# Kernel tuning notes

Hardware: AMD Instinct MI355X
Metric: run time of the kernel (lower is better)

The kernel has to match this reference:

```python
import jax, jax.numpy as jnp
import numpy as np

D_MODEL = 768
D_STATE = 128
D_CONV = 4
EXPAND = 2
HEADDIM = 64
NGROUPS = 1
D_INNER = EXPAND * D_MODEL            # 1536
NHEADS = D_INNER // HEADDIM           # 24
CONV_DIM = D_INNER + 2 * NGROUPS * D_STATE  # 1792
D_IN_PROJ = 2 * D_INNER + 2 * NGROUPS * D_STATE + NHEADS  # 3352
EPS = 1e-5


def setup_inputs() -> dict:
    key = jax.random.key(0)
    ks = jax.random.split(key, 8)
    b, l = 4, 2048
    return {
        "feature": jax.random.normal(ks[0], (b, l, D_MODEL), jnp.float32),
        "in_proj_w": jax.random.normal(ks[1], (D_IN_PROJ, D_MODEL), jnp.float32) * 0.02,
        "conv_w": jax.random.normal(ks[2], (CONV_DIM, D_CONV), jnp.float32) * 0.2,
        "conv_b": jnp.zeros((CONV_DIM,), jnp.float32),
        "dt_bias": jax.random.normal(ks[3], (NHEADS,), jnp.float32) * 0.1,
        # A in [1,16) -> A_log = log(A)
        "A_log": jnp.log(1.0 + 15.0 * jax.random.uniform(ks[4], (NHEADS,), jnp.float32)),
        "D": jnp.ones((NHEADS,), jnp.float32),
        "norm_w": jnp.ones((D_INNER,), jnp.float32),
        "out_proj_w": jax.random.normal(ks[5], (D_MODEL, D_INNER), jnp.float32) * 0.02,
        "gate1": jnp.float32(0.6),
    }


def _mamba2(u, in_proj_w, conv_w, conv_b, dt_bias, A_log, D, norm_w, out_proj_w):
    b, l, _ = u.shape
    zxbcdt = jnp.einsum('bld,ed->ble', u, in_proj_w)  # [b,l,3352]
    z, xBC, dt = jnp.split(zxbcdt, [D_INNER, D_INNER + CONV_DIM], axis=-1)
    dt = jax.nn.softplus(dt + dt_bias)  # [b,l,h]

    # causal depthwise conv1d + silu on xBC
    xc = jnp.transpose(xBC, (0, 2, 1))  # [b,c,l]
    xc = jax.lax.conv_general_dilated(
        xc, conv_w[:, None, :], (1,), [(D_CONV - 1, 0)],
        dimension_numbers=('NCH', 'OIH', 'NCH'), feature_group_count=CONV_DIM)
    xBC = jax.nn.silu(jnp.transpose(xc, (0, 2, 1)) + conv_b)

    x, B, C = jnp.split(xBC, [D_INNER, D_INNER + NGROUPS * D_STATE], axis=-1)
    x = x.reshape(b, l, NHEADS, HEADDIM)
    A = -jnp.exp(A_log)          # [h], negative
    dA = jnp.exp(dt * A)         # [b,l,h]

    def step(h, inp):
        # h: [b,h,p,n]
        dA_t, dt_t, x_t, B_t, C_t = inp  # [b,h],[b,h],[b,h,p],[b,n],[b,n]
        h = h * dA_t[..., None, None] + (dt_t[..., None] * x_t)[..., None] * B_t[:, None, None, :]
        y = jnp.einsum('bhpn,bn->bhp', h, C_t)
        return h, y

    h0 = jnp.zeros((b, NHEADS, HEADDIM, D_STATE), u.dtype)
    xs = (jnp.moveaxis(dA, 1, 0), jnp.moveaxis(dt, 1, 0), jnp.moveaxis(x, 1, 0),
          jnp.moveaxis(B, 1, 0), jnp.moveaxis(C, 1, 0))
    _, ys = jax.lax.scan(step, h0, xs)           # [l,b,h,p]
    y = jnp.moveaxis(ys, 0, 1) + x * D[None, None, :, None]
    y = y.reshape(b, l, D_INNER)

    # gated RMSNorm: gate then normalize (norm_before_gate=False)
    y = y * jax.nn.silu(z)
    y = y * jax.lax.rsqrt(jnp.mean(y * y, axis=-1, keepdims=True) + EPS) * norm_w
    return jnp.einsum('bld,ed->ble', y, out_proj_w)


def reference(feature, in_proj_w, conv_w, conv_b, dt_bias, A_log, D, norm_w, out_proj_w, gate1):
    out = _mamba2(feature, in_proj_w, conv_w, conv_b, dt_bias, A_log, D, norm_w, out_proj_w)
    return jax.nn.sigmoid(gate1) * out
```

## Files before the change

### kernel.cpp

```cpp
#include <hip/hip_runtime.h>
#include <cstddef>

#define NB 4
#define SEQL 2048
#define DMODEL 768
#define DSTATE 128
#define HEADDIM 64
#define NHEADS 24
#define DINNER 1536
#define CONVDIM 1792
#define DINPROJ 3352
#define BLROWS (NB*SEQL)
#define RMS_EPS 1e-5f
#define Q 128
#define NC (SEQL/Q)
#define BOFF DINNER
#define COFF (DINNER + DSTATE)
#define BK 64

typedef unsigned int uint;
typedef unsigned short ushort;
typedef __attribute__((ext_vector_type(8))) short bf16x8;
typedef __attribute__((ext_vector_type(4))) float f32x4;

__device__ __forceinline__ float sigmoidf_(float x){ return 1.f/(1.f+expf(-x)); }
__device__ __forceinline__ float siluf_(float x){ return x * sigmoidf_(x); }
__device__ __forceinline__ float softplusf_(float x){ return x > 20.f ? x : log1pf(expf(x)); }

__device__ __forceinline__ ushort f2bf(float f){
    union { float f; uint u; } v; v.f = f;
    uint r = (v.u + 0x7FFFu + ((v.u >> 16) & 1u)) >> 16;
    return (ushort)r;
}
__device__ __forceinline__ float bf2f(ushort s){
    union { uint u; float f; } v; v.u = ((uint)s) << 16;
    return v.f;
}
__device__ __forceinline__ uint pack2(float a, float b){
    return (uint)f2bf(a) | ((uint)f2bf(b) << 16);
}
__device__ __forceinline__ void unpack8(uint4 r, float* o){
    o[0]=bf2f((ushort)(r.x&0xffff)); o[1]=bf2f((ushort)(r.x>>16));
    o[2]=bf2f((ushort)(r.y&0xffff)); o[3]=bf2f((ushort)(r.y>>16));
    o[4]=bf2f((ushort)(r.z&0xffff)); o[5]=bf2f((ushort)(r.z>>16));
    o[6]=bf2f((ushort)(r.w&0xffff)); o[7]=bf2f((ushort)(r.w>>16));
}
__device__ __forceinline__ uint packu2(ushort a, ushort b){
    return (uint)a | ((uint)b << 16);
}

#define GLD16(g, l) __builtin_amdgcn_global_load_lds( \
    (const __attribute__((address_space(1))) void*)(g), \
    (__attribute__((address_space(3))) void*)(l), 16, 0, 0)

__global__ __launch_bounds__(256) void cast_kernel(
    const float* __restrict__ in, ushort* __restrict__ out, int n4)
{
    const int i = blockIdx.x*256 + threadIdx.x;
    if (i < n4) {
        float4 v = ((const float4*)in)[i];
        ushort4 o = make_ushort4(f2bf(v.x), f2bf(v.y), f2bf(v.z), f2bf(v.w));
        ((ushort4*)out)[i] = o;
    }
}

__global__ __launch_bounds__(256) void gemm_mfma(
    const ushort* __restrict__ A, const ushort* __restrict__ W,
    float* __restrict__ C, int M, int N, int K,
    const float* __restrict__ gptr)
{
    __shared__ __align__(16) ushort sm[2*12288];
    const int tid = threadIdx.x;
    const int wv = tid >> 6, ln = tid & 63;
    const int id = blockIdx.x;
    const int xcd = id & 7;
    const int local = id >> 3;
    const int m0 = (xcd*8 + (local & 7)) * 128;
    const int n0 = (local >> 3) * 64;
    const int wm = (wv >> 1) * 64, wn = (wv & 1) * 32;

    const int sr = ln >> 3;
    const int scol = ((ln & 7) ^ sr) * 8;
    const ushort* gA[4]; ushort* lA[4];
#pragma unroll
    for (int iss = 0; iss < 4; ++iss) {
        gA[iss] = A + (size_t)(m0 + wv*32 + iss*8 + sr) * K + scol;
        lA[iss] = &sm[(wv*32 + iss*8) * BK];
    }
    const ushort* gB[2]; ushort* lB[2];
#pragma unroll
    for (int iss = 0; iss < 2; ++iss) {
        gB[iss] = W + (size_t)(n0 + wv*16 + iss*8 + sr) * K + scol;
        lB[iss] = &sm[8192 + (wv*16 + iss*8) * BK];
    }

    f32x4 acc[4][2];
#pragma unroll
    for (int i = 0; i < 4; ++i)
#pragma unroll
        for (int j = 0; j < 2; ++j) acc[i][j] = (f32x4){0.f, 0.f, 0.f, 0.f};

    const int fr = ln & 15;
    const int fq = ln >> 4;
    const int nt = K / BK;

#pragma unroll
    for (int iss = 0; iss < 4; ++iss) GLD16(gA[iss], lA[iss]);
#pragma unroll
    for (int iss = 0; iss < 2; ++iss) GLD16(gB[iss], lB[iss]);

    for (int kt = 0; kt < nt; ++kt) {
        if (kt + 1 < nt) {
            const int so = ((kt + 1) & 1) * 12288;
            const int ko = (kt + 1) * BK;
#pragma unroll
            for (int iss = 0; iss < 4; ++iss) GLD16(gA[iss] + ko, lA[iss] + so);
#pragma unroll
            for (int iss = 0; iss < 2; ++iss) GLD16(gB[iss] + ko, lB[iss] + so);
            asm volatile("s_waitcnt vmcnt(6)" ::: "memory");
        } else {
            asm volatile("s_waitcnt vmcnt(0)" ::: "memory");
        }
        __builtin_amdgcn_s_barrier();
        const ushort* As = sm + (kt & 1) * 12288;
        const ushort* Bs = As + 8192;
#pragma unroll
        for (int kh = 0; kh < 2; ++kh) {
            const int sw = ((kh*4 + fq) ^ (fr & 7)) * 8;
            bf16x8 af[4], bfr[2];
#pragma unroll
            for (int i = 0; i < 4; ++i)
                af[i] = *(const bf16x8*)&As[(wm + i*16 + fr)*BK + sw];
#pragma unroll
            for (int j = 0; j < 2; ++j)
                bfr[j] = *(const bf16x8*)&Bs[(wn + j*16 + fr)*BK + sw];
#pragma unroll
            for (int i = 0; i < 4; ++i)
#pragma unroll
                for (int j = 0; j < 2; ++j)
                    acc[i][j] = __builtin_amdgcn_mfma_f32_16x16x32_bf16(af[i], bfr[j], acc[i][j], 0, 0, 0);
        }
        __builtin_amdgcn_s_barrier();
    }

    float scale = 1.f;
    if (gptr) scale = sigmoidf_(*gptr);
    const int cn = ln & 15;
    const int cr = (ln >> 4) * 4;
#pragma unroll
    for (int i = 0; i < 4; ++i) {
        const int mb = m0 + wm + i*16 + cr;
#pragma unroll
        for (int j = 0; j < 2; ++j) {
            const int n = n0 + wn + j*16 + cn;
            if (n < N) {
                float* cp = C + (size_t)mb * N + n;
                cp[0*(size_t)N] = acc[i][j].x * scale;
                cp[1*(size_t)N] = acc[i][j].y * scale;
                cp[2*(size_t)N] = acc[i][j].z * scale;
                cp[3*(size_t)N] = acc[i][j].w * scale;
            }
        }
    }
}

__global__ __launch_bounds__(256) void gemm_mfma_bf16o(
    const ushort* __restrict__ A, const ushort* __restrict__ W,
    ushort* __restrict__ C, float* __restrict__ dtraw, int M, int N, int K)
{
    __shared__ __align__(16) ushort sm[2*128*BK*2];
    const int tid = threadIdx.x;
    const int wv = tid >> 6, ln = tid & 63;
    const int id = blockIdx.x;
    const int xcd = id & 7;
    const int local = id >> 3;
    const int m0 = (xcd*8 + (local & 7)) * 128;
    const int n0 = (local >> 3) * 128;
    const int wm = (wv >> 1) * 64, wn = (wv & 1) * 64;

    const int sr = ln >> 3;
    const int scol = ((ln & 7) ^ sr) * 8;
    const ushort* gA[4]; const ushort* gB[4];
    ushort* lA[4]; ushort* lB[4];
#pragma unroll
    for (int iss = 0; iss < 4; ++iss) {
        const int ra = m0 + wv*32 + iss*8 + sr;
        gA[iss] = A + (size_t)ra * K + scol;
        int rb = n0 + wv*32 + iss*8 + sr; if (rb >= N) rb = N - 1;
        gB[iss] = W + (size_t)rb * K + scol;
        lA[iss] = &sm[(wv*32 + iss*8) * BK];
        lB[iss] = &sm[8192 + (wv*32 + iss*8) * BK];
    }

    f32x4 acc[4][4];
#pragma unroll
    for (int i = 0; i < 4; ++i)
#pragma unroll
        for (int j = 0; j < 4; ++j) acc[i][j] = (f32x4){0.f, 0.f, 0.f, 0.f};

    const int fr = ln & 15;
    const int fq = ln >> 4;
    const int nt = K / BK;

#pragma unroll
    for (int iss = 0; iss < 4; ++iss) {
        GLD16(gA[iss], lA[iss]);
        GLD16(gB[iss], lB[iss]);
    }

    for (int kt = 0; kt < nt; ++kt) {
        if (kt + 1 < nt) {
            const int so = ((kt + 1) & 1) * 16384;
            const int ko = (kt + 1) * BK;
#pragma unroll
            for (int iss = 0; iss < 4; ++iss) {
                GLD16(gA[iss] + ko, lA[iss] + so);
                GLD16(gB[iss] + ko, lB[iss] + so);
            }
            asm volatile("s_waitcnt vmcnt(8)" ::: "memory");
        } else {
            asm volatile("s_waitcnt vmcnt(0)" ::: "memory");
        }
        __builtin_amdgcn_s_barrier();
        const ushort* As = sm + (kt & 1) * 16384;
        const ushort* Bs = As + 8192;
#pragma unroll
        for (int kh = 0; kh < 2; ++kh) {
            const int sw = ((kh*4 + fq) ^ (fr & 7)) * 8;
            bf16x8 af[4], bfr[4];
#pragma unroll
            for (int i = 0; i < 4; ++i)
                af[i] = *(const bf16x8*)&As[(wm + i*16 + fr)*BK + sw];
#pragma unroll
            for (int j = 0; j < 4; ++j)
                bfr[j] = *(const bf16x8*)&Bs[(wn + j*16 + fr)*BK + sw];
#pragma unroll
            for (int i = 0; i < 4; ++i)
#pragma unroll
                for (int j = 0; j < 4; ++j)
                    acc[i][j] = __builtin_amdgcn_mfma_f32_16x16x32_bf16(af[i], bfr[j], acc[i][j], 0, 0, 0);
        }
        __builtin_amdgcn_s_barrier();
    }

    const int cn = ln & 15;
    const int cr = (ln >> 4) * 4;
    __syncthreads();
    ushort* rp = sm + wv*4096;
#pragma unroll
    for (int i = 0; i < 4; ++i)
#pragma unroll
        for (int j = 0; j < 4; ++j) {
            const int colb = j*16 + cn;
#pragma unroll
            for (int r = 0; r < 4; ++r) {
                const int row = i*16 + cr + r;
                rp[row*64 + (((colb >> 3) ^ (row & 7)) * 8) + (colb & 7)] = f2bf(acc[i][j][r]);
            }
        }
    __syncthreads();
#pragma unroll
    for (int k2 = 0; k2 < 8; ++k2) {
        const int row = k2*8 + (ln >> 3);
        const int cg = ln & 7;
        uint4 v = *(const uint4*)&rp[row*64 + ((cg ^ (row & 7)) * 8)];
        const int gm = m0 + wm + row;
        const int gn = n0 + wn + cg*8;
        if (gn + 8 <= N)
            *(uint4*)(C + (size_t)gm*N + gn) = v;
    }
    if (n0 + 128 > N) {
#pragma unroll
        for (int i = 0; i < 4; ++i) {
            const int mb = m0 + wm + i*16 + cr;
#pragma unroll
            for (int j = 0; j < 4; ++j) {
                const int col = (n0 + wn + j*16 + cn) - (N - 24);
                if (col >= 0 && col < 24) {
                    dtraw[(size_t)(mb+0)*24 + col] = acc[i][j].x;
                    dtraw[(size_t)(mb+1)*24 + col] = acc[i][j].y;
                    dtraw[(size_t)(mb+2)*24 + col] = acc[i][j].z;
                    dtraw[(size_t)(mb+3)*24 + col] = acc[i][j].w;
                }
            }
        }
    }
}

__global__ __launch_bounds__(448) void conv_kernel(
    const ushort* __restrict__ zx, const float* __restrict__ conv_w,
    const float* __restrict__ conv_b, ushort* __restrict__ xconv)
{
    const int c4 = threadIdx.x;
    const int bl0 = blockIdx.x * 16;
    const int l0 = bl0 & (SEQL - 1);
    float w[4][4];
#pragma unroll
    for (int j = 0; j < 4; ++j) {
        float4 wr = *(const float4*)(conv_w + (c4*4 + j)*4);
        w[j][0]=wr.x; w[j][1]=wr.y; w[j][2]=wr.z; w[j][3]=wr.w;
    }
    const float4 bias = *(const float4*)(conv_b + c4*4);
    const ushort* src = zx + DINNER + (size_t)c4*4;
    ushort* dst = xconv + (size_t)c4*4;

    float h0[4], h1[4], h2[4];
    if (l0 == 0) {
#pragma unroll
        for (int ch = 0; ch < 4; ++ch) { h0[ch]=0.f; h1[ch]=0.f; h2[ch]=0.f; }
    } else {
        ushort4 a = *(const ushort4*)(src + (size_t)(bl0-3)*DINPROJ);
        ushort4 b = *(const ushort4*)(src + (size_t)(bl0-2)*DINPROJ);
        ushort4 c = *(const ushort4*)(src + (size_t)(bl0-1)*DINPROJ);
        h0[0]=bf2f(a.x); h0[1]=bf2f(a.y); h0[2]=bf2f(a.z); h0[3]=bf2f(a.w);
        h1[0]=bf2f(b.x); h1[1]=bf2f(b.y); h1[2]=bf2f(b.z); h1[3]=bf2f(b.w);
        h2[0]=bf2f(c.x); h2[1]=bf2f(c.y); h2[2]=bf2f(c.z); h2[3]=bf2f(c.w);
    }
#pragma unroll
    for (int t = 0; t < 16; ++t) {
        ushort4 xv = *(const ushort4*)(src + (size_t)(bl0 + t)*DINPROJ);
        float h3[4] = {bf2f(xv.x), bf2f(xv.y), bf2f(xv.z), bf2f(xv.w)};
        float s0 = fmaf(h3[0], w[0][3], fmaf(h2[0], w[0][2], fmaf(h1[0], w[0][1], fmaf(h0[0], w[0][0], bias.x))));
        float s1 = fmaf(h3[1], w[1][3], fmaf(h2[1], w[1][2], fmaf(h1[1], w[1][1], fmaf(h0[1], w[1][0], bias.y))));
        float s2 = fmaf(h3[2], w[2][3], fmaf(h2[2], w[2][2], fmaf(h1[2], w[2][1], fmaf(h0[2], w[2][0], bias.z))));
        float s3 = fmaf(h3[3], w[3][3], fmaf(h2[3], w[3][2], fmaf(h1[3], w[3][1], fmaf(h0[3], w[3][0], bias.w))));
        ushort4 o = make_ushort4(f2bf(siluf_(s0)), f2bf(siluf_(s1)),
                                 f2bf(siluf_(s2)), f2bf(siluf_(s3)));
        *(ushort4*)(dst + (size_t)(bl0 + t)*CONVDIM) = o;
#pragma unroll
        for (int ch = 0; ch < 4; ++ch) { h0[ch]=h1[ch]; h1[ch]=h2[ch]; h2[ch]=h3[ch]; }
    }
}

__global__ __launch_bounds__(128) void dtscan_kernel(
    const float* __restrict__ dtraw, const float* __restrict__ dt_bias,
    const float* __restrict__ A_log, float* __restrict__ dtc, float* __restrict__ clog)
{
    const int c = blockIdx.x, h = blockIdx.y, b = blockIdx.z;
    const int t = threadIdx.x;
    const int bl = b*SEQL + c*Q + t;
    float draw = dtraw[(size_t)bl*24 + h] + dt_bias[h];
    float dtv = softplusf_(draw);
    float la = -expf(A_log[h]) * dtv;
    const int lane = t & 63;
    float v = la;
#pragma unroll
    for (int off = 1; off < 64; off <<= 1) {
        float u = __shfl_up(v, off);
        if (lane >= off) v += u;
    }
    __shared__ float w0tot;
    if (t == 63) w0tot = v;
    __syncthreads();
    if (t >= 64) v += w0tot;
    const int idx = (b*NHEADS + h)*SEQL + c*Q + t;
    dtc[idx] = dtv;
    clog[idx] = v;
}

__global__ __launch_bounds__(256) void gcb_mfma(
    const ushort* __restrict__ xconv, ushort* __restrict__ G)
{
    __shared__ __align__(16) ushort Ca[64*32];
    __shared__ __align__(16) ushort Bb[128*32];
    const int thalf = blockIdx.x, c = blockIdx.y, b = blockIdx.z;
    const int tid = threadIdx.x;
    const int wv = tid >> 6, ln = tid & 63;
    const int fr = ln & 15, fq = ln >> 4, fk = fq*8;
    const int bl0 = b*SEQL + c*Q;
    const int th0 = thalf*64;

    const int sat = tid & 63,  sac = (tid >> 6)*8;
    const int sbt = tid & 127, sbh = (tid >> 7)*16;

    f32x4 acc[4][2];
#pragma unroll
    for (int i = 0; i < 4; ++i)
#pragma unroll
        for (int j = 0; j < 2; ++j) acc[i][j] = (f32x4){0.f,0.f,0.f,0.f};

    for (int ks = 0; ks < 4; ++ks) {
        uint4 av = *(const uint4*)(xconv + (size_t)(bl0 + th0 + sat)*CONVDIM + COFF + ks*32 + sac);
        const ushort* br = xconv + (size_t)(bl0 + sbt)*CONVDIM + BOFF + ks*32 + sbh;
        uint4 bv0 = *(const uint4*)br;
        uint4 bv1 = *(const uint4*)(br + 8);
        __syncthreads();
        *(uint4*)&Ca[sat*32 + sac] = av;
        *(uint4*)&Bb[sbt*32 + sbh] = bv0;
        *(uint4*)&Bb[sbt*32 + sbh + 8] = bv1;
        __syncthreads();
        bf16x8 av_[4], bv_[2];
#pragma unroll
        for (int i = 0; i < 4; ++i)
            av_[i] = *(const bf16x8*)&Ca[(i*16 + fr)*32 + fk];
#pragma unroll
        for (int j = 0; j < 2; ++j)
            bv_[j] = *(const bf16x8*)&Bb[(wv*32 + j*16 + fr)*32 + fk];
#pragma unroll
        for (int i = 0; i < 4; ++i)
#pragma unroll
            for (int j = 0; j < 2; ++j)
                acc[i][j] = __builtin_amdgcn_mfma_f32_16x16x32_bf16(av_[i], bv_[j], acc[i][j], 0, 0, 0);
    }
    ushort* gout = G + (size_t)(b*NC + c)*(Q*Q);
#pragma unroll
    for (int i = 0; i < 4; ++i) {
#pragma unroll
        for (int j = 0; j < 2; ++j) {
            const int s = wv*32 + j*16 + fr;
#pragma unroll
            for (int r = 0; r < 4; ++r) {
                const int t = th0 + i*16 + fq*4 + r;
                gout[t*Q + s] = f2bf(acc[i][j][r]);
            }
        }
    }
}

#define ASTR 40
#define BSTR 40
__global__ __launch_bounds__(256) void locstate_mfma(
    const ushort* __restrict__ xconv, const float* __restrict__ dtc,
    const float* __restrict__ clog, ushort* __restrict__ Sloc)
{
    __shared__ __align__(16) ushort Ab[64*ASTR];
    __shared__ __align__(16) ushort Bb[128*BSTR];
    __shared__ float sw[Q];
    const int c = blockIdx.x, h = blockIdx.y, b = blockIdx.z;
    const int tid = threadIdx.x;
    const int wv = tid >> 6, ln = tid & 63;
    const int fr = ln & 15, fq = ln >> 4, fk = fq*8;
    const int bh = b*NHEADS + h;
    const int bl0 = b*SEQL + c*Q;

    if (tid < Q) {
        const float ce = clog[(size_t)bh*SEQL + c*Q + (Q-1)];
        const float cs = clog[(size_t)bh*SEQL + c*Q + tid];
        sw[tid] = dtc[(size_t)bh*SEQL + c*Q + tid] * expf(ce - cs);
    }
    __syncthreads();

    f32x4 acc[4][2];
#pragma unroll
    for (int i = 0; i < 4; ++i)
#pragma unroll
        for (int j = 0; j < 2; ++j) acc[i][j] = (f32x4){0.f,0.f,0.f,0.f};

    const int ap = tid & 63, aoct = tid >> 6;
    const int bn = tid & 127, bhalf = tid >> 7;

    for (int ks = 0; ks < 4; ++ks) {
        float xv[8];
#pragma unroll
        for (int j = 0; j < 8; ++j) {
            const int s = ks*32 + aoct*8 + j;
            xv[j] = bf2f(xconv[(size_t)(bl0 + s)*CONVDIM + h*HEADDIM + ap]) * sw[s];
        }
        ushort bu[16];
#pragma unroll
        for (int j = 0; j < 16; ++j) {
            const int s = ks*32 + bhalf*16 + j;
            bu[j] = xconv[(size_t)(bl0 + s)*CONVDIM + BOFF + bn];
        }
        __syncthreads();
        *(uint4*)&Ab[ap*ASTR + aoct*8] =
            make_uint4(pack2(xv[0],xv[1]), pack2(xv[2],xv[3]),
                       pack2(xv[4],xv[5]), pack2(xv[6],xv[7]));
        *(uint4*)&Bb[bn*BSTR + bhalf*16] =
            make_uint4(packu2(bu[0],bu[1]), packu2(bu[2],bu[3]),
                       packu2(bu[4],bu[5]), packu2(bu[6],bu[7]));
        *(uint4*)&Bb[bn*BSTR + bhalf*16 + 8] =
            make_uint4(packu2(bu[8],bu[9]), packu2(bu[10],bu[11]),
                       packu2(bu[12],bu[13]), packu2(bu[14],bu[15]));
        __syncthreads();
        bf16x8 af[4], bf[2];
#pragma unroll
        for (int i = 0; i < 4; ++i)
            af[i] = *(const bf16x8*)&Ab[(i*16 + fr)*ASTR + fk];
#pragma unroll
        for (int j = 0; j < 2; ++j)
            bf[j] = *(const bf16x8*)&Bb[(wv*32 + j*16 + fr)*BSTR + fk];
#pragma unroll
        for (int i = 0; i < 4; ++i)
#pragma unroll
            for (int j = 0; j < 2; ++j)
                acc[i][j] = __builtin_amdgcn_mfma_f32_16x16x32_bf16(af[i], bf[j], acc[i][j], 0, 0, 0);
    }
    ushort* dst = Sloc + (size_t)((b*NC + c)*NHEADS + h) * (HEADDIM*DSTATE);
#pragma unroll
    for (int i = 0; i < 4; ++i) {
#pragma unroll
        for (int j = 0; j < 2; ++j) {
            const int n = wv*32 + j*16 + fr;
#pragma unroll
            for (int r = 0; r < 4; ++r) {
                const int p = i*16 + fq*4 + r;
                dst[p*DSTATE + n] = f2bf(acc[i][j][r]);
            }
        }
    }
}

__global__ __launch_bounds__(256) void chunkscan_kernel(
    const float* __restrict__ clog, ushort* __restrict__ S)
{
    const int h = blockIdx.x, b = blockIdx.y, pg = blockIdx.z;
    const int tid = threadIdx.x;
    const int p = pg*16 + (tid >> 4);
    const int n0 = (tid & 15) * 8;
    const int bh = b*NHEADS + h;
    float st[8];
#pragma unroll
    for (int j = 0; j < 8; ++j) st[j] = 0.f;

    for (int c = 0; c < NC; ++c) {
        const float tc = expf(clog[(size_t)bh*SEQL + c*Q + (Q-1)]);
        ushort* base = S + (size_t)((b*NC + c)*NHEADS + h) * (HEADDIM*DSTATE);
        uint4 raw = *(uint4*)(base + p*DSTATE + n0);
        float lv[8];
        unpack8(raw, lv);
        uint4 pre = make_uint4(pack2(st[0],st[1]), pack2(st[2],st[3]),
                               pack2(st[4],st[5]), pack2(st[6],st[7]));
        *(uint4*)(base + p*DSTATE + n0) = pre;
#pragma unroll
        for (int j = 0; j < 8; ++j) st[j] = fmaf(tc, st[j], lv[j]);
    }
}

__global__ __launch_bounds__(256) void ychunk_mfma(
    const ushort* __restrict__ xconv, const float* __restrict__ dtc,
    const float* __restrict__ clog, const ushort* __restrict__ G,
    const ushort* __restrict__ Sp, const float* __restrict__ Dv,
    ushort* __restrict__ ybf)
{
    __shared__ __align__(16) ushort smu[8192];
    ushort* Ab = smu;
    ushort* Bb = smu + 4096;
    __shared__ float s_clog[Q];
    __shared__ float s_dtc[Q];
    const int c = blockIdx.x, h = blockIdx.y, b = blockIdx.z;
    const int tid = threadIdx.x;
    const int wv = tid >> 6, ln = tid & 63;
    const int bh = b*NHEADS + h;
    const int bl0 = b*SEQL + c*Q;
    const int fr = ln & 15, fq = ln >> 4, fk = fq*8;

    if (tid < Q) {
        s_clog[tid] = clog[(size_t)bh*SEQL + c*Q + tid];
        s_dtc[tid]  = dtc [(size_t)bh*SEQL + c*Q + tid];
    }

    f32x4 acc[2][4];
#pragma unroll
    for (int i = 0; i < 2; ++i)
#pragma unroll
        for (int j = 0; j < 4; ++j) acc[i][j] = (f32x4){0.f,0.f,0.f,0.f};

    const int sgt = tid & 127, sgh = (tid >> 7)*16;
    const int sbp = tid & 63,  sbc = (tid >> 6)*8;
    const ushort* spb = Sp + (size_t)((b*NC + c)*NHEADS + h)*(HEADDIM*DSTATE);

    for (int ks = 0; ks < 4; ++ks) {
        const ushort* cr = xconv + (size_t)(bl0 + sgt)*CONVDIM + COFF + ks*32 + sgh;
        uint4 cv0 = *(const uint4*)cr;
        uint4 cv1 = *(const uint4*)(cr + 8);
        uint4 sv = *(const uint4*)(spb + sbp*DSTATE + ks*32 + sbc);
        __syncthreads();
        *(uint4*)&Ab[sgt*32 + sgh]     = cv0;
        *(uint4*)&Ab[sgt*32 + sgh + 8] = cv1;
        *(uint4*)&Bb[sbp*32 + sbc] = sv;
        __syncthreads();
        bf16x8 af[2], bv[4];
        af[0] = *(const bf16x8*)&Ab[(wv*32 +      fr)*32 + fk];
        af[1] = *(const bf16x8*)&Ab[(wv*32 + 16 + fr)*32 + fk];
#pragma unroll
        for (int j = 0; j < 4; ++j)
            bv[j] = *(const bf16x8*)&Bb[(j*16 + fr)*32 + fk];
#pragma unroll
        for (int i = 0; i < 2; ++i)
#pragma unroll
            for (int j = 0; j < 4; ++j)
                acc[i][j] = __builtin_amdgcn_mfma_f32_16x16x32_bf16(af[i], bv[j], acc[i][j], 0, 0, 0);
    }
#pragma unroll
    for (int i = 0; i < 2; ++i) {
        const int tb = wv*32 + i*16 + fq*4;
        float e0 = expf(s_clog[tb+0]), e1 = expf(s_clog[tb+1]);
        float e2 = expf(s_clog[tb+2]), e3 = expf(s_clog[tb+3]);
#pragma unroll
        for (int j = 0; j < 4; ++j) {
            acc[i][j].x *= e0; acc[i][j].y *= e1; acc[i][j].z *= e2; acc[i][j].w *= e3;
        }
    }

    const ushort* gp = G + (size_t)(b*NC + c)*(Q*Q);
    for (int ks = 0; ks < 4; ++ks) {
        uint4 g0 = *(const uint4*)(gp + sgt*Q + ks*32 + sgh);
        uint4 g1 = *(const uint4*)(gp + sgt*Q + ks*32 + sgh + 8);
        ushort xu[8];
#pragma unroll
        for (int j = 0; j < 8; ++j)
            xu[j] = xconv[(size_t)(bl0 + ks*32 + sbc + j)*CONVDIM + h*HEADDIM + sbp];
        __syncthreads();
        {
            float gvals[16];
            unpack8(g0, gvals);
            unpack8(g1, gvals + 8);
            const float ct = s_clog[sgt];
            ushort gw[16];
#pragma unroll
            for (int j = 0; j < 16; ++j) {
                const int s = ks*32 + sgh + j;
                float w = 0.f;
                if (s <= sgt) w = s_dtc[s] * expf(ct - s_clog[s]);
                gw[j] = f2bf(gvals[j] * w);
            }
            *(uint4*)&Ab[sgt*32 + sgh] =
                make_uint4(packu2(gw[0],gw[1]), packu2(gw[2],gw[3]),
                           packu2(gw[4],gw[5]), packu2(gw[6],gw[7]));
            *(uint4*)&Ab[sgt*32 + sgh + 8] =
                make_uint4(packu2(gw[8],gw[9]), packu2(gw[10],gw[11]),
                           packu2(gw[12],gw[13]), packu2(gw[14],gw[15]));
            *(uint4*)&Bb[sbp*32 + sbc] =
                make_uint4(packu2(xu[0],xu[1]), packu2(xu[2],xu[3]),
                           packu2(xu[4],xu[5]), packu2(xu[6],xu[7]));
        }
        __syncthreads();
        if (ks <= wv) {
            bf16x8 af[2], bv[4];
            af[0] = *(const bf16x8*)&Ab[(wv*32 +      fr)*32 + fk];
            af[1] = *(const bf16x8*)&Ab[(wv*32 + 16 + fr)*32 + fk];
#pragma unroll
            for (int j = 0; j < 4; ++j)
                bv[j] = *(const bf16x8*)&Bb[(j*16 + fr)*32 + fk];
#pragma unroll
            for (int i = 0; i < 2; ++i)
#pragma unroll
                for (int j = 0; j < 4; ++j)
                    acc[i][j] = __builtin_amdgcn_mfma_f32_16x16x32_bf16(af[i], bv[j], acc[i][j], 0, 0, 0);
        }
    }

    const float Dh = Dv[h];
    __syncthreads();
    ushort* rp = smu;
#pragma unroll
    for (int i = 0; i < 2; ++i) {
#pragma unroll
        for (int r = 0; r < 4; ++r) {
            const int t = wv*32 + i*16 + fq*4 + r;
            const ushort* xr = xconv + (size_t)(bl0 + t)*CONVDIM + h*HEADDIM;
#pragma unroll
            for (int j = 0; j < 4; ++j) {
                const int p = j*16 + fr;
                rp[t*64 + p] = f2bf(acc[i][j][r] + Dh * bf2f(xr[p]));
            }
        }
    }
#pragma unroll
    for (int k2 = 0; k2 < 4; ++k2) {
        const int row = wv*32 + k2*8 + (ln >> 3);
        uint4 v = *(const uint4*)&rp[row*64 + (ln & 7)*8];
        *(uint4*)(ybf + (size_t)(bl0 + row)*DINNER + h*HEADDIM + (ln & 7)*8) = v;
    }
}

__global__ __launch_bounds__(128) void rms_kernel(
    const ushort* __restrict__ zx, const float* __restrict__ norm_w,
    ushort* __restrict__ ybf)
{
    const int row = blockIdx.x;
    const int tid = threadIdx.x;
    const ushort* zr = zx + (size_t)row * DINPROJ;
    ushort* yr = ybf + (size_t)row * DINNER;
    float v[12];
    float ss = 0.f;
#pragma unroll
    for (int i = 0; i < 3; ++i) {
        const int o = (tid + i*128) * 4;
        ushort4 yv = *(const ushort4*)(yr + o);
        ushort4 zv = *(const ushort4*)(zr + o);
        float a = bf2f(yv.x) * siluf_(bf2f(zv.x));
        float b = bf2f(yv.y) * siluf_(bf2f(zv.y));
        float cc = bf2f(yv.z) * siluf_(bf2f(zv.z));
        float d = bf2f(yv.w) * siluf_(bf2f(zv.w));
        v[i*4+0]=a; v[i*4+1]=b; v[i*4+2]=cc; v[i*4+3]=d;
        ss += a*a + b*b + cc*cc + d*d;
    }
#pragma unroll
    for (int off = 1; off < 64; off <<= 1) ss += __shfl_xor(ss, off);
    __shared__ float red[2];
    if ((tid & 63) == 0) red[tid >> 6] = ss;
    __syncthreads();
    const float rstd = rsqrtf((red[0] + red[1]) * (1.f/DINNER) + RMS_EPS);
#pragma unroll
    for (int i = 0; i < 3; ++i) {
        const int o = (tid + i*128) * 4;
        float4 wv = *(const float4*)(norm_w + o);
        ushort4 ov = make_ushort4(f2bf(v[i*4+0]*rstd*wv.x), f2bf(v[i*4+1]*rstd*wv.y),
                                  f2bf(v[i*4+2]*rstd*wv.z), f2bf(v[i*4+3]*rstd*wv.w));
        *(ushort4*)(yr + o) = ov;
    }
}

extern "C" void kernel_launch(void* const* d_in, const int* in_sizes, int n_in,
                              void* d_out, int out_size, void* d_ws, size_t ws_size,
                              hipStream_t stream)
{
    const float* feature    = (const float*)d_in[0];
    const float* in_proj_w  = (const float*)d_in[1];
    const float* conv_w     = (const float*)d_in[2];
    const float* conv_b     = (const float*)d_in[3];
    const float* dt_bias    = (const float*)d_in[4];
    const float* A_log      = (const float*)d_in[5];
    const float* Dvec       = (const float*)d_in[6];
    const float* norm_w     = (const float*)d_in[7];
    const float* out_proj_w = (const float*)d_in[8];
    const float* gate1      = (const float*)d_in[9];
    float* out = (float*)d_out;

    ushort* zx    = (ushort*)d_ws;
    ushort* xconv = zx + (size_t)BLROWS * DINPROJ;
    ushort* ybf   = xconv + (size_t)BLROWS * CONVDIM;
    float* dtraw  = (float*)(ybf + (size_t)BLROWS * DINNER);
    float* dtc    = dtraw + (size_t)BLROWS * 24;
    float* clog   = dtc + (size_t)NB * NHEADS * SEQL;
    ushort* Gbuf  = (ushort*)(clog + (size_t)NB * NHEADS * SEQL);
    ushort* Sbuf  = Gbuf + (size_t)NB * NC * Q * Q;
    ushort* Abf    = Gbuf;
    ushort* Wbf_in = Gbuf + (size_t)BLROWS * DMODEL;
    ushort* Wbf_out = zx;

    cast_kernel<<<dim3((BLROWS*DMODEL/4 + 255)/256), 256, 0, stream>>>(feature, Abf, BLROWS*DMODEL/4);
    cast_kernel<<<dim3((DINPROJ*DMODEL/4 + 255)/256), 256, 0, stream>>>(in_proj_w, Wbf_in, DINPROJ*DMODEL/4);
    gemm_mfma_bf16o<<<dim3(27*64), 256, 0, stream>>>(Abf, Wbf_in, zx, dtraw,
                                                     BLROWS, DINPROJ, DMODEL);
    conv_kernel<<<dim3(BLROWS/16), 448, 0, stream>>>(zx, conv_w, conv_b, xconv);
    dtscan_kernel<<<dim3(NC, NHEADS, NB), 128, 0, stream>>>(dtraw, dt_bias, A_log, dtc, clog);
    gcb_mfma<<<dim3(2, NC, NB), 256, 0, stream>>>(xconv, Gbuf);
    locstate_mfma<<<dim3(NC, NHEADS, NB), 256, 0, stream>>>(xconv, dtc, clog, Sbuf);
    chunkscan_kernel<<<dim3(NHEADS, NB, 4), 256, 0, stream>>>(clog, Sbuf);
    ychunk_mfma<<<dim3(NC, NHEADS, NB), 256, 0, stream>>>(xconv, dtc, clog, Gbuf, Sbuf, Dvec, ybf);
    rms_kernel<<<dim3(BLROWS), 128, 0, stream>>>(zx, norm_w, ybf);
    cast_kernel<<<dim3((DMODEL*DINNER/4 + 255)/256), 256, 0, stream>>>(out_proj_w, Wbf_out, DMODEL*DINNER/4);
    gemm_mfma<<<dim3(768), 256, 0, stream>>>(ybf, Wbf_out, out,
                                             BLROWS, DMODEL, DINNER, gate1);
}
```

Baseline: 285.8 us.

## Enlarge in-projection GEMM to 256x256 tiles with 8 waves and staged prefetch

```diff
diff --git a/kernel.cpp b/kernel.cpp
--- a/kernel.cpp
+++ b/kernel.cpp
@@ -53,6 +53,8 @@
     (const __attribute__((address_space(1))) void*)(g), \
     (__attribute__((address_space(3))) void*)(l), 16, 0, 0)
 
+#define MFMA_BF16(a, b, c) __builtin_amdgcn_mfma_f32_16x16x32_bf16((a), (b), (c), 0, 0, 0)
+
 __global__ __launch_bounds__(256) void cast_kernel(
     const float* __restrict__ in, ushort* __restrict__ out, int n4)
 {
@@ -138,7 +140,7 @@
             for (int i = 0; i < 4; ++i)
 #pragma unroll
                 for (int j = 0; j < 2; ++j)
-                    acc[i][j] = __builtin_amdgcn_mfma_f32_16x16x32_bf16(af[i], bfr[j], acc[i][j], 0, 0, 0);
+                    acc[i][j] = MFMA_BF16(af[i], bfr[j], acc[i][j]);
         }
         __builtin_amdgcn_s_barrier();
     }
@@ -164,91 +166,129 @@
     }
 }
 
-__global__ __launch_bounds__(256) void gemm_mfma_bf16o(
+__global__ __launch_bounds__(512) void gemm_mfma_bf16o(
     const ushort* __restrict__ A, const ushort* __restrict__ W,
     ushort* __restrict__ C, float* __restrict__ dtraw, int M, int N, int K)
 {
-    __shared__ __align__(16) ushort sm[2*128*BK*2];
+    __shared__ __align__(16) ushort sm[65536];
     const int tid = threadIdx.x;
     const int wv = tid >> 6, ln = tid & 63;
     const int id = blockIdx.x;
     const int xcd = id & 7;
     const int local = id >> 3;
-    const int m0 = (xcd*8 + (local & 7)) * 128;
-    const int n0 = (local >> 3) * 128;
-    const int wm = (wv >> 1) * 64, wn = (wv & 1) * 64;
-
-    const int sr = ln >> 3;
-    const int scol = ((ln & 7) ^ sr) * 8;
-    const ushort* gA[4]; const ushort* gB[4];
-    ushort* lA[4]; ushort* lB[4];
-#pragma unroll
-    for (int iss = 0; iss < 4; ++iss) {
-        const int ra = m0 + wv*32 + iss*8 + sr;
-        gA[iss] = A + (size_t)ra * K + scol;
-        int rb = n0 + wv*32 + iss*8 + sr; if (rb >= N) rb = N - 1;
-        gB[iss] = W + (size_t)rb * K + scol;
-        lA[iss] = &sm[(wv*32 + iss*8) * BK];
-        lB[iss] = &sm[8192 + (wv*32 + iss*8) * BK];
-    }
-
-    f32x4 acc[4][4];
-#pragma unroll
-    for (int i = 0; i < 4; ++i)
+    const int m0 = (xcd*4 + (local & 3)) * 256;
+    const int n0 = (local >> 2) * 256;
+    const int wm = (wv >> 2) * 128, wn = (wv & 3) * 64;
+
+    const int srow = tid >> 3;
+    const int scg  = ((tid & 7) ^ (srow & 7)) * 8;
+    const ushort* gSA[2][2];
+    const ushort* gSB[2][2];
+#pragma unroll
+    for (int h = 0; h < 2; ++h)
+#pragma unroll
+        for (int r = 0; r < 2; ++r) {
+            gSA[h][r] = A + (size_t)(m0 + h*128 + r*64 + srow) * K + scg;
+            int rb = n0 + h*128 + r*64 + srow; if (rb >= N) rb = N - 1;
+            gSB[h][r] = W + (size_t)rb * K + scg;
+        }
+    char* smb = (char*)sm;
+    const int wvb = wv * 1024;
+#define STA8(kt,h,r) GLD16(gSA[h][r] + (size_t)(kt)*BK, smb + (((kt)&1)*32768 + (h)*16384 + (r)*8192 + wvb))
+#define STB8(kt,h,r) GLD16(gSB[h][r] + (size_t)(kt)*BK, smb + (65536 + ((kt)&1)*32768 + (h)*16384 + (r)*8192 + wvb))
+
+    f32x4 acc[8][4];
+#pragma unroll
+    for (int i = 0; i < 8; ++i)
 #pragma unroll
         for (int j = 0; j < 4; ++j) acc[i][j] = (f32x4){0.f, 0.f, 0.f, 0.f};
 
     const int fr = ln & 15;
     const int fq = ln >> 4;
     const int nt = K / BK;
-
-#pragma unroll
-    for (int iss = 0; iss < 4; ++iss) {
-        GLD16(gA[iss], lA[iss]);
-        GLD16(gB[iss], lB[iss]);
-    }
-
-    for (int kt = 0; kt < nt; ++kt) {
-        if (kt + 1 < nt) {
-            const int so = ((kt + 1) & 1) * 16384;
-            const int ko = (kt + 1) * BK;
-#pragma unroll
-            for (int iss = 0; iss < 4; ++iss) {
-                GLD16(gA[iss] + ko, lA[iss] + so);
-                GLD16(gB[iss] + ko, lB[iss] + so);
-            }
-            asm volatile("s_waitcnt vmcnt(8)" ::: "memory");
-        } else {
-            asm volatile("s_waitcnt vmcnt(0)" ::: "memory");
-        }
-        __builtin_amdgcn_s_barrier();
-        const ushort* As = sm + (kt & 1) * 16384;
-        const ushort* Bs = As + 8192;
-#pragma unroll
-        for (int kh = 0; kh < 2; ++kh) {
-            const int sw = ((kh*4 + fq) ^ (fr & 7)) * 8;
-            bf16x8 af[4], bfr[4];
-#pragma unroll
-            for (int i = 0; i < 4; ++i)
-                af[i] = *(const bf16x8*)&As[(wm + i*16 + fr)*BK + sw];
-#pragma unroll
-            for (int j = 0; j < 4; ++j)
-                bfr[j] = *(const bf16x8*)&Bs[(wn + j*16 + fr)*BK + sw];
-#pragma unroll
-            for (int i = 0; i < 4; ++i)
-#pragma unroll
-                for (int j = 0; j < 4; ++j)
-                    acc[i][j] = __builtin_amdgcn_mfma_f32_16x16x32_bf16(af[i], bfr[j], acc[i][j], 0, 0, 0);
-        }
+#define FRA8(i,kh) (*(const bf16x8*)&As[(wm + (i)*16 + fr)*64 + ((((kh)*4 + fq) ^ (fr & 7))*8)])
+#define FRB8(j,kh) (*(const bf16x8*)&Bs[(wn + (j)*16 + fr)*64 + ((((kh)*4 + fq) ^ (fr & 7))*8)])
+
+#pragma unroll
+    for (int h = 0; h < 2; ++h) { STB8(0,h,0); STB8(0,h,1); }
+#pragma unroll
+    for (int h = 0; h < 2; ++h) { STA8(0,h,0); STA8(0,h,1); }
+#pragma unroll
+    for (int h = 0; h < 2; ++h) { STB8(1,h,0); STB8(1,h,1); }
+    asm volatile("s_waitcnt vmcnt(4)" ::: "memory");
+    __builtin_amdgcn_s_barrier();
+
+    for (int u = 0; u < nt; ++u) {
+        const ushort* As = sm + (u & 1) * 16384;
+        const ushort* Bs = sm + 32768 + (u & 1) * 16384;
+        bf16x8 bfr[4][2];
+        bf16x8 a0h0, a0h1, a1h0, a1h1;
+
+#pragma unroll
+        for (int j = 0; j < 4; ++j) { bfr[j][0] = FRB8(j,0); bfr[j][1] = FRB8(j,1); }
+        a0h0 = FRA8(0,0); a0h1 = FRA8(0,1); a1h0 = FRA8(1,0); a1h1 = FRA8(1,1);
+        if (u + 1 < nt) { STA8(u+1,0,0); STA8(u+1,0,1); STA8(u+1,1,0); STA8(u+1,1,1); }
+        __builtin_amdgcn_s_barrier();
+        __builtin_amdgcn_s_setprio(1);
+#pragma unroll
+        for (int j = 0; j < 4; ++j) {
+            acc[0][j] = MFMA_BF16(a0h0, bfr[j][0], acc[0][j]);
+            acc[0][j] = MFMA_BF16(a0h1, bfr[j][1], acc[0][j]);
+            acc[1][j] = MFMA_BF16(a1h0, bfr[j][0], acc[1][j]);
+            acc[1][j] = MFMA_BF16(a1h1, bfr[j][1], acc[1][j]);
+        }
+        __builtin_amdgcn_s_setprio(0);
+        __builtin_amdgcn_s_barrier();
+
+        a0h0 = FRA8(2,0); a0h1 = FRA8(2,1); a1h0 = FRA8(3,0); a1h1 = FRA8(3,1);
+        __builtin_amdgcn_s_barrier();
+        __builtin_amdgcn_s_setprio(1);
+#pragma unroll
+        for (int j = 0; j < 4; ++j) {
+            acc[2][j] = MFMA_BF16(a0h0, bfr[j][0], acc[2][j]);
+            acc[2][j] = MFMA_BF16(a0h1, bfr[j][1], acc[2][j]);
+            acc[3][j] = MFMA_BF16(a1h0, bfr[j][0], acc[3][j]);
+            acc[3][j] = MFMA_BF16(a1h1, bfr[j][1], acc[3][j]);
+        }
+        __builtin_amdgcn_s_setprio(0);
+        __builtin_amdgcn_s_barrier();
+
+        a0h0 = FRA8(4,0); a0h1 = FRA8(4,1); a1h0 = FRA8(5,0); a1h1 = FRA8(5,1);
+        if (u + 2 < nt) { STB8(u+2,0,0); STB8(u+2,0,1); STB8(u+2,1,0); STB8(u+2,1,1); }
+        __builtin_amdgcn_s_barrier();
+        __builtin_amdgcn_s_setprio(1);
+#pragma unroll
+        for (int j = 0; j < 4; ++j) {
+            acc[4][j] = MFMA_BF16(a0h0, bfr[j][0], acc[4][j]);
+            acc[4][j] = MFMA_BF16(a0h1, bfr[j][1], acc[4][j]);
+            acc[5][j] = MFMA_BF16(a1h0, bfr[j][0], acc[5][j]);
+            acc[5][j] = MFMA_BF16(a1h1, bfr[j][1], acc[5][j]);
+        }
+        __builtin_amdgcn_s_setprio(0);
+        __builtin_amdgcn_s_barrier();
+
+        a0h0 = FRA8(6,0); a0h1 = FRA8(6,1); a1h0 = FRA8(7,0); a1h1 = FRA8(7,1);
+        __builtin_amdgcn_s_barrier();
+        __builtin_amdgcn_s_setprio(1);
+#pragma unroll
+        for (int j = 0; j < 4; ++j) {
+            acc[6][j] = MFMA_BF16(a0h0, bfr[j][0], acc[6][j]);
+            acc[6][j] = MFMA_BF16(a0h1, bfr[j][1], acc[6][j]);
+            acc[7][j] = MFMA_BF16(a1h0, bfr[j][0], acc[7][j]);
+            acc[7][j] = MFMA_BF16(a1h1, bfr[j][1], acc[7][j]);
+        }
+        __builtin_amdgcn_s_setprio(0);
+        if (u + 2 < nt)      { asm volatile("s_waitcnt vmcnt(4)" ::: "memory"); }
+        else if (u + 1 < nt) { asm volatile("s_waitcnt vmcnt(0)" ::: "memory"); }
         __builtin_amdgcn_s_barrier();
     }
 
     const int cn = ln & 15;
     const int cr = (ln >> 4) * 4;
     __syncthreads();
-    ushort* rp = sm + wv*4096;
-#pragma unroll
-    for (int i = 0; i < 4; ++i)
+    ushort* rp = sm + wv*8192;
+#pragma unroll
+    for (int i = 0; i < 8; ++i)
 #pragma unroll
         for (int j = 0; j < 4; ++j) {
             const int colb = j*16 + cn;
@@ -260,7 +300,7 @@
         }
     __syncthreads();
 #pragma unroll
-    for (int k2 = 0; k2 < 8; ++k2) {
+    for (int k2 = 0; k2 < 16; ++k2) {
         const int row = k2*8 + (ln >> 3);
         const int cg = ln & 7;
         uint4 v = *(const uint4*)&rp[row*64 + ((cg ^ (row & 7)) * 8)];
@@ -269,9 +309,9 @@
         if (gn + 8 <= N)
             *(uint4*)(C + (size_t)gm*N + gn) = v;
     }
-    if (n0 + 128 > N) {
-#pragma unroll
-        for (int i = 0; i < 4; ++i) {
+    if (n0 + 256 > N) {
+#pragma unroll
+        for (int i = 0; i < 8; ++i) {
             const int mb = m0 + wm + i*16 + cr;
 #pragma unroll
             for (int j = 0; j < 4; ++j) {
@@ -285,6 +325,10 @@
             }
         }
     }
+#undef STA8
+#undef STB8
+#undef FRA8
+#undef FRB8
 }
 
 __global__ __launch_bounds__(448) void conv_kernel(
@@ -400,7 +444,7 @@
         for (int i = 0; i < 4; ++i)
 #pragma unroll
             for (int j = 0; j < 2; ++j)
-                acc[i][j] = __builtin_amdgcn_mfma_f32_16x16x32_bf16(av_[i], bv_[j], acc[i][j], 0, 0, 0);
+                acc[i][j] = MFMA_BF16(av_[i], bv_[j], acc[i][j]);
     }
     ushort* gout = G + (size_t)(b*NC + c)*(Q*Q);
 #pragma unroll
@@ -484,7 +528,7 @@
         for (int i = 0; i < 4; ++i)
 #pragma unroll
             for (int j = 0; j < 2; ++j)
-                acc[i][j] = __builtin_amdgcn_mfma_f32_16x16x32_bf16(af[i], bf[j], acc[i][j], 0, 0, 0);
+                acc[i][j] = MFMA_BF16(af[i], bf[j], acc[i][j]);
     }
     ushort* dst = Sloc + (size_t)((b*NC + c)*NHEADS + h) * (HEADDIM*DSTATE);
 #pragma unroll
@@ -580,7 +624,7 @@
         for (int i = 0; i < 2; ++i)
 #pragma unroll
             for (int j = 0; j < 4; ++j)
-                acc[i][j] = __builtin_amdgcn_mfma_f32_16x16x32_bf16(af[i], bv[j], acc[i][j], 0, 0, 0);
+                acc[i][j] = MFMA_BF16(af[i], bv[j], acc[i][j]);
     }
 #pragma unroll
     for (int i = 0; i < 2; ++i) {
@@ -637,7 +681,7 @@
             for (int i = 0; i < 2; ++i)
 #pragma unroll
                 for (int j = 0; j < 4; ++j)
-                    acc[i][j] = __builtin_amdgcn_mfma_f32_16x16x32_bf16(af[i], bv[j], acc[i][j], 0, 0, 0);
+                    acc[i][j] = MFMA_BF16(af[i], bv[j], acc[i][j]);
         }
     }
 
@@ -733,8 +777,8 @@
 
     cast_kernel<<<dim3((BLROWS*DMODEL/4 + 255)/256), 256, 0, stream>>>(feature, Abf, BLROWS*DMODEL/4);
     cast_kernel<<<dim3((DINPROJ*DMODEL/4 + 255)/256), 256, 0, stream>>>(in_proj_w, Wbf_in, DINPROJ*DMODEL/4);
-    gemm_mfma_bf16o<<<dim3(27*64), 256, 0, stream>>>(Abf, Wbf_in, zx, dtraw,
-                                                     BLROWS, DINPROJ, DMODEL);
+    gemm_mfma_bf16o<<<dim3(448), 512, 0, stream>>>(Abf, Wbf_in, zx, dtraw,
+                                                   BLROWS, DINPROJ, DMODEL);
     conv_kernel<<<dim3(BLROWS/16), 448, 0, stream>>>(zx, conv_w, conv_b, xconv);
     dtscan_kernel<<<dim3(NC, NHEADS, NB), 128, 0, stream>>>(dtraw, dt_bias, A_log, dtc, clog);
     gcb_mfma<<<dim3(2, NC, NB), 256, 0, stream>>>(xconv, Gbuf);
```

Result: no change. 290.7 us (+1.7%).

## Prefetch next k-slice into registers in SSD kernels and use fast exp

Applied to the files above, without the earlier changes.

```diff
diff --git a/kernel.cpp b/kernel.cpp
--- a/kernel.cpp
+++ b/kernel.cpp
@@ -23,9 +23,10 @@
 typedef __attribute__((ext_vector_type(8))) short bf16x8;
 typedef __attribute__((ext_vector_type(4))) float f32x4;
 
-__device__ __forceinline__ float sigmoidf_(float x){ return 1.f/(1.f+expf(-x)); }
+__device__ __forceinline__ float fexp_(float x){ return __expf(x); }
+__device__ __forceinline__ float sigmoidf_(float x){ return 1.f/(1.f+__expf(-x)); }
 __device__ __forceinline__ float siluf_(float x){ return x * sigmoidf_(x); }
-__device__ __forceinline__ float softplusf_(float x){ return x > 20.f ? x : log1pf(expf(x)); }
+__device__ __forceinline__ float softplusf_(float x){ return x > 20.f ? x : log1pf(__expf(x)); }
 
 __device__ __forceinline__ ushort f2bf(float f){
     union { float f; uint u; } v; v.f = f;
@@ -52,6 +53,8 @@
 #define GLD16(g, l) __builtin_amdgcn_global_load_lds( \
     (const __attribute__((address_space(1))) void*)(g), \
     (__attribute__((address_space(3))) void*)(l), 16, 0, 0)
+
+#define MFMA_BF16(a, b, c) __builtin_amdgcn_mfma_f32_16x16x32_bf16((a), (b), (c), 0, 0, 0)
 
 __global__ __launch_bounds__(256) void cast_kernel(
     const float* __restrict__ in, ushort* __restrict__ out, int n4)
@@ -138,7 +141,7 @@
             for (int i = 0; i < 4; ++i)
 #pragma unroll
                 for (int j = 0; j < 2; ++j)
-                    acc[i][j] = __builtin_amdgcn_mfma_f32_16x16x32_bf16(af[i], bfr[j], acc[i][j], 0, 0, 0);
+                    acc[i][j] = MFMA_BF16(af[i], bfr[j], acc[i][j]);
         }
         __builtin_amdgcn_s_barrier();
     }
@@ -238,7 +241,7 @@
             for (int i = 0; i < 4; ++i)
 #pragma unroll
                 for (int j = 0; j < 4; ++j)
-                    acc[i][j] = __builtin_amdgcn_mfma_f32_16x16x32_bf16(af[i], bfr[j], acc[i][j], 0, 0, 0);
+                    acc[i][j] = MFMA_BF16(af[i], bfr[j], acc[i][j]);
         }
         __builtin_amdgcn_s_barrier();
     }
@@ -341,7 +344,7 @@
     const int bl = b*SEQL + c*Q + t;
     float draw = dtraw[(size_t)bl*24 + h] + dt_bias[h];
     float dtv = softplusf_(draw);
-    float la = -expf(A_log[h]) * dtv;
+    float la = -fexp_(A_log[h]) * dtv;
     const int lane = t & 63;
     float v = la;
 #pragma unroll
@@ -400,7 +403,7 @@
         for (int i = 0; i < 4; ++i)
 #pragma unroll
             for (int j = 0; j < 2; ++j)
-                acc[i][j] = __builtin_amdgcn_mfma_f32_16x16x32_bf16(av_[i], bv_[j], acc[i][j], 0, 0, 0);
+                acc[i][j] = MFMA_BF16(av_[i], bv_[j], acc[i][j]);
     }
     ushort* gout = G + (size_t)(b*NC + c)*(Q*Q);
 #pragma unroll
@@ -436,9 +439,8 @@
     if (tid < Q) {
         const float ce = clog[(size_t)bh*SEQL + c*Q + (Q-1)];
         const float cs = clog[(size_t)bh*SEQL + c*Q + tid];
-        sw[tid] = dtc[(size_t)bh*SEQL + c*Q + tid] * expf(ce - cs);
-    }
-    __syncthreads();
+        sw[tid] = dtc[(size_t)bh*SEQL + c*Q + tid] * fexp_(ce - cs);
+    }
 
     f32x4 acc[4][2];
 #pragma unroll
@@ -449,29 +451,40 @@
     const int ap = tid & 63, aoct = tid >> 6;
     const int bn = tid & 127, bhalf = tid >> 7;
 
+    ushort xrc[8]; ushort buc[16];
+#pragma unroll
+    for (int j = 0; j < 8; ++j)
+        xrc[j] = xconv[(size_t)(bl0 + aoct*8 + j)*CONVDIM + h*HEADDIM + ap];
+#pragma unroll
+    for (int j = 0; j < 16; ++j)
+        buc[j] = xconv[(size_t)(bl0 + bhalf*16 + j)*CONVDIM + BOFF + bn];
+
+#pragma unroll
     for (int ks = 0; ks < 4; ++ks) {
-        float xv[8];
-#pragma unroll
-        for (int j = 0; j < 8; ++j) {
-            const int s = ks*32 + aoct*8 + j;
-            xv[j] = bf2f(xconv[(size_t)(bl0 + s)*CONVDIM + h*HEADDIM + ap]) * sw[s];
-        }
-        ushort bu[16];
-#pragma unroll
-        for (int j = 0; j < 16; ++j) {
-            const int s = ks*32 + bhalf*16 + j;
-            bu[j] = xconv[(size_t)(bl0 + s)*CONVDIM + BOFF + bn];
-        }
         __syncthreads();
-        *(uint4*)&Ab[ap*ASTR + aoct*8] =
-            make_uint4(pack2(xv[0],xv[1]), pack2(xv[2],xv[3]),
-                       pack2(xv[4],xv[5]), pack2(xv[6],xv[7]));
-        *(uint4*)&Bb[bn*BSTR + bhalf*16] =
-            make_uint4(packu2(bu[0],bu[1]), packu2(bu[2],bu[3]),
-                       packu2(bu[4],bu[5]), packu2(bu[6],bu[7]));
-        *(uint4*)&Bb[bn*BSTR + bhalf*16 + 8] =
-            make_uint4(packu2(bu[8],bu[9]), packu2(bu[10],bu[11]),
-                       packu2(bu[12],bu[13]), packu2(bu[14],bu[15]));
+        {
+            float xv[8];
+#pragma unroll
+            for (int j = 0; j < 8; ++j)
+                xv[j] = bf2f(xrc[j]) * sw[ks*32 + aoct*8 + j];
+            *(uint4*)&Ab[ap*ASTR + aoct*8] =
+                make_uint4(pack2(xv[0],xv[1]), pack2(xv[2],xv[3]),
+                           pack2(xv[4],xv[5]), pack2(xv[6],xv[7]));
+            *(uint4*)&Bb[bn*BSTR + bhalf*16] =
+                make_uint4(packu2(buc[0],buc[1]), packu2(buc[2],buc[3]),
+                           packu2(buc[4],buc[5]), packu2(buc[6],buc[7]));
+            *(uint4*)&Bb[bn*BSTR + bhalf*16 + 8] =
+                make_uint4(packu2(buc[8],buc[9]), packu2(buc[10],buc[11]),
+                           packu2(buc[12],buc[13]), packu2(buc[14],buc[15]));
+        }
+        if (ks < 3) {
+#pragma unroll
+            for (int j = 0; j < 8; ++j)
+                xrc[j] = xconv[(size_t)(bl0 + (ks+1)*32 + aoct*8 + j)*CONVDIM + h*HEADDIM + ap];
+#pragma unroll
+            for (int j = 0; j < 16; ++j)
+                buc[j] = xconv[(size_t)(bl0 + (ks+1)*32 + bhalf*16 + j)*CONVDIM + BOFF + bn];
+        }
         __syncthreads();
         bf16x8 af[4], bf[2];
 #pragma unroll
@@ -484,7 +497,7 @@
         for (int i = 0; i < 4; ++i)
 #pragma unroll
             for (int j = 0; j < 2; ++j)
-                acc[i][j] = __builtin_amdgcn_mfma_f32_16x16x32_bf16(af[i], bf[j], acc[i][j], 0, 0, 0);
+                acc[i][j] = MFMA_BF16(af[i], bf[j], acc[i][j]);
     }
     ushort* dst = Sloc + (size_t)((b*NC + c)*NHEADS + h) * (HEADDIM*DSTATE);
 #pragma unroll
@@ -513,12 +526,15 @@
 #pragma unroll
     for (int j = 0; j < 8; ++j) st[j] = 0.f;
 
+    uint4 raw = *(uint4*)(S + (size_t)((b*NC + 0)*NHEADS + h) * (HEADDIM*DSTATE) + p*DSTATE + n0);
     for (int c = 0; c < NC; ++c) {
-        const float tc = expf(clog[(size_t)bh*SEQL + c*Q + (Q-1)]);
+        uint4 cur = raw;
         ushort* base = S + (size_t)((b*NC + c)*NHEADS + h) * (HEADDIM*DSTATE);
-        uint4 raw = *(uint4*)(base + p*DSTATE + n0);
+        if (c + 1 < NC)
+            raw = *(uint4*)(S + (size_t)((b*NC + c + 1)*NHEADS + h) * (HEADDIM*DSTATE) + p*DSTATE + n0);
+        const float tc = fexp_(clog[(size_t)bh*SEQL + c*Q + (Q-1)]);
         float lv[8];
-        unpack8(raw, lv);
+        unpack8(cur, lv);
         uint4 pre = make_uint4(pack2(st[0],st[1]), pack2(st[2],st[3]),
                                pack2(st[4],st[5]), pack2(st[6],st[7]));
         *(uint4*)(base + p*DSTATE + n0) = pre;
@@ -560,15 +576,21 @@
     const int sbp = tid & 63,  sbc = (tid >> 6)*8;
     const ushort* spb = Sp + (size_t)((b*NC + c)*NHEADS + h)*(HEADDIM*DSTATE);
 
+    uint4 cv0c = *(const uint4*)(xconv + (size_t)(bl0 + sgt)*CONVDIM + COFF + sgh);
+    uint4 cv1c = *(const uint4*)(xconv + (size_t)(bl0 + sgt)*CONVDIM + COFF + sgh + 8);
+    uint4 svc  = *(const uint4*)(spb + sbp*DSTATE + sbc);
+#pragma unroll
     for (int ks = 0; ks < 4; ++ks) {
-        const ushort* cr = xconv + (size_t)(bl0 + sgt)*CONVDIM + COFF + ks*32 + sgh;
-        uint4 cv0 = *(const uint4*)cr;
-        uint4 cv1 = *(const uint4*)(cr + 8);
-        uint4 sv = *(const uint4*)(spb + sbp*DSTATE + ks*32 + sbc);
         __syncthreads();
-        *(uint4*)&Ab[sgt*32 + sgh]     = cv0;
-        *(uint4*)&Ab[sgt*32 + sgh + 8] = cv1;
-        *(uint4*)&Bb[sbp*32 + sbc] = sv;
+        *(uint4*)&Ab[sgt*32 + sgh]     = cv0c;
+        *(uint4*)&Ab[sgt*32 + sgh + 8] = cv1c;
+        *(uint4*)&Bb[sbp*32 + sbc] = svc;
+        if (ks < 3) {
+            const ushort* cr = xconv + (size_t)(bl0 + sgt)*CONVDIM + COFF + (ks+1)*32 + sgh;
+            cv0c = *(const uint4*)cr;
+            cv1c = *(const uint4*)(cr + 8);
+            svc  = *(const uint4*)(spb + sbp*DSTATE + (ks+1)*32 + sbc);
+        }
         __syncthreads();
         bf16x8 af[2], bv[4];
         af[0] = *(const bf16x8*)&Ab[(wv*32 +      fr)*32 + fk];
@@ -580,39 +602,42 @@
         for (int i = 0; i < 2; ++i)
 #pragma unroll
             for (int j = 0; j < 4; ++j)
-                acc[i][j] = __builtin_amdgcn_mfma_f32_16x16x32_bf16(af[i], bv[j], acc[i][j], 0, 0, 0);
-    }
+                acc[i][j] = MFMA_BF16(af[i], bv[j], acc[i][j]);
+    }
+
+    const ushort* gp = G + (size_t)(b*NC + c)*(Q*Q);
+    uint4 g0c = *(const uint4*)(gp + sgt*Q + sgh);
+    uint4 g1c = *(const uint4*)(gp + sgt*Q + sgh + 8);
+    ushort xuc[8];
+#pragma unroll
+    for (int j = 0; j < 8; ++j)
+        xuc[j] = xconv[(size_t)(bl0 + sbc + j)*CONVDIM + h*HEADDIM + sbp];
+
 #pragma unroll
     for (int i = 0; i < 2; ++i) {
         const int tb = wv*32 + i*16 + fq*4;
-        float e0 = expf(s_clog[tb+0]), e1 = expf(s_clog[tb+1]);
-        float e2 = expf(s_clog[tb+2]), e3 = expf(s_clog[tb+3]);
+        float e0 = fexp_(s_clog[tb+0]), e1 = fexp_(s_clog[tb+1]);
+        float e2 = fexp_(s_clog[tb+2]), e3 = fexp_(s_clog[tb+3]);
 #pragma unroll
         for (int j = 0; j < 4; ++j) {
             acc[i][j].x *= e0; acc[i][j].y *= e1; acc[i][j].z *= e2; acc[i][j].w *= e3;
         }
     }
 
-    const ushort* gp = G + (size_t)(b*NC + c)*(Q*Q);
+#pragma unroll
     for (int ks = 0; ks < 4; ++ks) {
-        uint4 g0 = *(const uint4*)(gp + sgt*Q + ks*32 + sgh);
-        uint4 g1 = *(const uint4*)(gp + sgt*Q + ks*32 + sgh + 8);
-        ushort xu[8];
-#pragma unroll
-        for (int j = 0; j < 8; ++j)
-            xu[j] = xconv[(size_t)(bl0 + ks*32 + sbc + j)*CONVDIM + h*HEADDIM + sbp];
         __syncthreads();
         {
             float gvals[16];
-            unpack8(g0, gvals);
-            unpack8(g1, gvals + 8);
+            unpack8(g0c, gvals);
+            unpack8(g1c, gvals + 8);
             const float ct = s_clog[sgt];
             ushort gw[16];
 #pragma unroll
             for (int j = 0; j < 16; ++j) {
                 const int s = ks*32 + sgh + j;
                 float w = 0.f;
-                if (s <= sgt) w = s_dtc[s] * expf(ct - s_clog[s]);
+                if (s <= sgt) w = s_dtc[s] * fexp_(ct - s_clog[s]);
                 gw[j] = f2bf(gvals[j] * w);
             }
             *(uint4*)&Ab[sgt*32 + sgh] =
@@ -622,8 +647,15 @@
                 make_uint4(packu2(gw[8],gw[9]), packu2(gw[10],gw[11]),
                            packu2(gw[12],gw[13]), packu2(gw[14],gw[15]));
             *(uint4*)&Bb[sbp*32 + sbc] =
-                make_uint4(packu2(xu[0],xu[1]), packu2(xu[2],xu[3]),
-                           packu2(xu[4],xu[5]), packu2(xu[6],xu[7]));
+                make_uint4(packu2(xuc[0],xuc[1]), packu2(xuc[2],xuc[3]),
+                           packu2(xuc[4],xuc[5]), packu2(xuc[6],xuc[7]));
+        }
+        if (ks < 3) {
+            g0c = *(const uint4*)(gp + sgt*Q + (ks+1)*32 + sgh);
+            g1c = *(const uint4*)(gp + sgt*Q + (ks+1)*32 + sgh + 8);
+#pragma unroll
+            for (int j = 0; j < 8; ++j)
+                xuc[j] = xconv[(size_t)(bl0 + (ks+1)*32 + sbc + j)*CONVDIM + h*HEADDIM + sbp];
         }
         __syncthreads();
         if (ks <= wv) {
@@ -637,7 +669,7 @@
             for (int i = 0; i < 2; ++i)
 #pragma unroll
                 for (int j = 0; j < 4; ++j)
-                    acc[i][j] = __builtin_amdgcn_mfma_f32_16x16x32_bf16(af[i], bv[j], acc[i][j], 0, 0, 0);
+                    acc[i][j] = MFMA_BF16(af[i], bv[j], acc[i][j]);
         }
     }
 
```

Measured after the change: 275.4 us. 1.04x faster.
